# Performance work log

Hardware: AMD Instinct MI355X
Metric: run time of the kernel (lower is better)

Reference implementation:

```python
import jax, jax.numpy as jnp
import numpy as np

N_CLUSTERS = 64
COLLAPSE_REG = 0.1
H_SMOOTH = -0.0001
H_ALPHA = 0.0001
H_LAMBDA = 0.0001


def setup_inputs() -> dict:
    key = jax.random.key(0)
    ks = jax.random.split(key, 6)
    n, d, k = 65536, 512, N_CLUSTERS
    e0 = 1048576  # directed edges before symmetrization
    features = jax.random.normal(ks[0], (n, d), jnp.float32)
    s = jax.random.randint(ks[1], (e0,), 0, n)
    t = jax.random.randint(ks[2], (e0,), 0, n)
    v = jax.random.uniform(ks[3], (e0,), jnp.float32)
    # symmetrize adjacency (real graph datasets are undirected -> L = D - A is PSD)
    edge_src = jnp.concatenate([s, t]).astype(jnp.int64)
    edge_dst = jnp.concatenate([t, s]).astype(jnp.int64)
    edge_vals = jnp.concatenate([v, v])
    W = jax.random.normal(ks[4], (d, k), jnp.float32) / np.sqrt(d).astype(np.float32)
    b = jnp.zeros((k,), jnp.float32)
    return dict(features=features, edge_src=edge_src, edge_dst=edge_dst,
                edge_vals=edge_vals, W=W, b=b)


def reference(features, edge_src, edge_dst, edge_vals, W, b):
    n, d = features.shape
    k = W.shape[1]
    # assignments = softmax(Dense(features))
    S = jax.nn.softmax(features @ W + b, axis=1)  # [n,k]
    cluster_sizes = jnp.sum(S, axis=0)            # [k]
    S_pool = S / cluster_sizes                    # [n,k]
    # sparse column-degree (tf.sparse.reduce_sum axis=0) and edge count
    deg_col = jax.ops.segment_sum(edge_vals, edge_dst, num_segments=n)[:, None]  # [n,1]
    m = jnp.sum(deg_col)
    # A @ S via edge-list gather/scatter (sparse_dense_matmul)
    AS = jax.ops.segment_sum(edge_vals[:, None] * S[edge_dst], edge_src,
                             num_segments=n)      # [n,k]
    graph_pooled = AS.T @ S                       # S^T A S, [k,k]
    normalizer = ((S.T @ deg_col) @ (deg_col.T @ S)) / 2.0 / m  # [k,k]
    spectral_loss = -jnp.trace(graph_pooled - normalizer) / 2.0 / m
    collapse_loss = (jnp.linalg.norm(cluster_sizes) / n
                     * jnp.sqrt(jnp.float32(k)) - 1.0)
    # pooled features
    FP = jax.nn.selu(S_pool.T @ features)         # [k,d]
    # FGC loss chain: Laplacian L = D_row - A applied sparsely
    deg_row = jax.ops.segment_sum(edge_vals, edge_src, num_segments=n)[:, None]
    LS = deg_row * S - AS                         # L @ S, [n,k]
    StLS = LS.T @ S                               # smoothness1 = S^T L S, [k,k]
    # log(det(StLS + ones)) computed stably via slogdet (det is positive: PSD + rank-1)
    _sign, logabsdet = jnp.linalg.slogdet(StLS + jnp.ones_like(StLS))
    smoothness_loss = logabsdet * H_SMOOTH
    # trace((L S) @ FP @ FP^T): trace of [n,k] matrix = sum of first k diagonal entries
    trace_loss = jnp.einsum('ic,cd,id->', LS[:k], FP, FP)
    frob_loss = jnp.linalg.norm(S @ FP - features) * H_ALPHA
    one_two_loss = jnp.linalg.norm(jnp.sum(jnp.abs(S), axis=0)) * H_LAMBDA
    fgc_loss = smoothness_loss + trace_loss + frob_loss + one_two_loss
    total_loss = spectral_loss + COLLAPSE_REG * collapse_loss + fgc_loss
    return FP, S, total_loss
```

## Files before the change

kernel.cpp:

```cpp
#include <hip/hip_runtime.h>
#include <hip/hip_bf16.h>
#include <cstdint>
#include <cstddef>

typedef unsigned short u16;
typedef float f32x4 __attribute__((ext_vector_type(4)));
typedef short bf16x8 __attribute__((ext_vector_type(8)));
typedef unsigned short u16x8 __attribute__((ext_vector_type(8)));

__device__ __forceinline__ u16 f2bf(float f) {
    uint32_t u = __float_as_uint(f);
    u += 0x7fffu + ((u >> 16) & 1u);
    return (u16)(u >> 16);
}
__device__ __forceinline__ float bf2f(u16 h) {
    return __uint_as_float(((uint32_t)h) << 16);
}

#define SWZ(c) ((((c) ^ ((c) >> 3)) & 7) << 2)

__global__ __launch_bounds__(256) void k_prep(const float* __restrict__ Wg, u16* __restrict__ Wt) {
    int idx = blockIdx.x * 256 + threadIdx.x;
    int k = idx >> 6, c = idx & 63;
    int lin = c * 512 + (k ^ ((c & 7) << 3));
    Wt[lin] = f2bf(Wg[idx]);
}

__global__ __launch_bounds__(256) void k1(const float* __restrict__ F,
    const u16* __restrict__ WtG, const float* __restrict__ bias,
    float* __restrict__ S_out, u16* __restrict__ Sbf,
    float* __restrict__ sizes, float* __restrict__ scal) {
    __shared__ __align__(16) u16 Wl[64 * 512];
    __shared__ __align__(16) u16 Al[64 * 64];
    __shared__ float red4[4];
    const int tid = threadIdx.x;
    const int row0 = blockIdx.x * 64;
    for (int j = tid; j < 4096; j += 256)
        ((uint4*)Wl)[j] = ((const uint4*)WtG)[j];

    const int lane = tid & 63;
    const int wv = __builtin_amdgcn_readfirstlane(tid >> 6);
    const int l15 = lane & 15, lq = lane >> 4;
    f32x4 acc[4];
    #pragma unroll
    for (int tn = 0; tn < 4; tn++)
        #pragma unroll
        for (int e = 0; e < 4; e++) acc[tn][e] = 0.f;
    float sumf2 = 0.f;
    const int sr = tid >> 2, skq = tid & 3;
    const int sw = (sr & 7) << 3;

    for (int k0 = 0; k0 < 512; k0 += 64) {
        const float* fp = F + (size_t)(row0 + sr) * 512 + k0 + skq * 16;
        float4 v[4];
        u16 h[16];
        #pragma unroll
        for (int q = 0; q < 4; q++) v[q] = ((const float4*)fp)[q];
        #pragma unroll
        for (int q = 0; q < 4; q++) {
            sumf2 += v[q].x * v[q].x + v[q].y * v[q].y + v[q].z * v[q].z + v[q].w * v[q].w;
            h[q * 4 + 0] = f2bf(v[q].x); h[q * 4 + 1] = f2bf(v[q].y);
            h[q * 4 + 2] = f2bf(v[q].z); h[q * 4 + 3] = f2bf(v[q].w);
        }
        #pragma unroll
        for (int half = 0; half < 2; half++) {
            u16x8 pk;
            #pragma unroll
            for (int e2 = 0; e2 < 8; e2++) pk[e2] = h[half * 8 + e2];
            *(u16x8*)&Al[sr * 64 + ((skq * 16 + half * 8) ^ sw)] = pk;
        }
        __syncthreads();
        #pragma unroll
        for (int kk = 0; kk < 64; kk += 32) {
            const int arow = wv * 16 + l15;
            bf16x8 a = *(const bf16x8*)&Al[arow * 64 + ((kk + lq * 8) ^ ((arow & 7) << 3))];
            #pragma unroll
            for (int tn = 0; tn < 4; tn++) {
                const int bc = tn * 16 + l15;
                bf16x8 b = *(const bf16x8*)&Wl[bc * 512 + ((k0 + kk + lq * 8) ^ ((bc & 7) << 3))];
                acc[tn] = __builtin_amdgcn_mfma_f32_16x16x32_bf16(a, b, acc[tn], 0, 0, 0);
            }
        }
        __syncthreads();
    }

    float bias4[4], szacc[4] = {0.f, 0.f, 0.f, 0.f};
    #pragma unroll
    for (int tn = 0; tn < 4; tn++) bias4[tn] = bias[tn * 16 + l15];
    #pragma unroll
    for (int r2 = 0; r2 < 4; r2++) {
        float L[4];
        #pragma unroll
        for (int tn = 0; tn < 4; tn++) L[tn] = acc[tn][r2] + bias4[tn];
        float mx = fmaxf(fmaxf(L[0], L[1]), fmaxf(L[2], L[3]));
        #pragma unroll
        for (int mm = 1; mm < 16; mm <<= 1) mx = fmaxf(mx, __shfl_xor(mx, mm));
        float e[4], s = 0.f;
        #pragma unroll
        for (int tn = 0; tn < 4; tn++) { e[tn] = __expf(L[tn] - mx); s += e[tn]; }
        #pragma unroll
        for (int mm = 1; mm < 16; mm <<= 1) s += __shfl_xor(s, mm);
        const float inv = 1.f / s;
        const size_t grow = (size_t)(row0 + wv * 16 + lq * 4 + r2);
        #pragma unroll
        for (int tn = 0; tn < 4; tn++) {
            const float svl = e[tn] * inv;
            S_out[grow * 64 + tn * 16 + l15] = svl;
            Sbf[grow * 64 + tn * 16 + l15] = f2bf(svl);
            szacc[tn] += svl;
        }
    }
    #pragma unroll
    for (int tn = 0; tn < 4; tn++) {
        float vs = szacc[tn];
        vs += __shfl_xor(vs, 16);
        vs += __shfl_xor(vs, 32);
        if (lq == 0) atomicAdd(sizes + tn * 16 + l15, vs);
    }
    #pragma unroll
    for (int mm = 1; mm < 64; mm <<= 1) sumf2 += __shfl_xor(sumf2, mm);
    if (lane == 0) red4[wv] = sumf2;
    __syncthreads();
    if (tid == 0) atomicAdd(scal + 1, red4[0] + red4[1] + red4[2] + red4[3]);
}

__global__ __launch_bounds__(512) void k_sweep(const int* __restrict__ esrc,
    const int* __restrict__ edst, const float* __restrict__ ev,
    const u16* __restrict__ Sbf, const float* __restrict__ S, const int E2,
    float* __restrict__ GP8, float* __restrict__ SDS8, float* __restrict__ uv8,
    float* __restrict__ AS64, float* __restrict__ deg64, float* __restrict__ scal) {
    __shared__ uint32_t Tl[2][2048];
    __shared__ uint32_t Pl[2][2048];
    __shared__ uint32_t Ql[2][2048];
    __shared__ uint32_t Rl[2][2048];
    const int tid = threadIdx.x;
    const int lane = tid & 63;
    const int wv = __builtin_amdgcn_readfirstlane(tid >> 6);
    const int l15 = lane & 15, lq = lane >> 4;
    const int xcd = blockIdx.x & 7;
    float* __restrict__ GPmy = GP8 + (size_t)xcd * 4096;
    float* __restrict__ SDSmy = SDS8 + (size_t)xcd * 4096;
    float* __restrict__ umy = uv8 + (size_t)xcd * 64;

    const bool isP = tid < 256;
    const int st = tid & 255;
    const int p = st >> 3, g = st & 7;
    float vsum = 0.f;
    float uacc[8];
    #pragma unroll
    for (int j = 0; j < 8; j++) uacc[j] = 0.f;

    f32x4 aG[2], aS[2];
    #pragma unroll
    for (int t = 0; t < 2; t++)
        #pragma unroll
        for (int r = 0; r < 4; r++) { aG[t][r] = 0.f; aS[t][r] = 0.f; }

    const int ma = 16 * (wv & 3) + l15;
    const int aoff = ma * 32, aswz = SWZ(ma);
    const int nb0 = 32 * (wv >> 2) + l15;
    const int nb1 = nb0 + 16;
    const int b0off = nb0 * 32, b0swz = SWZ(nb0);
    const int b1off = nb1 * 32, b1swz = SWZ(nb1);

    const int nch = E2 >> 6;
    const int stride = gridDim.x;
    int ch = blockIdx.x;
    if (ch >= nch) return;

    int2 ia_c, ib_c, ia_n, ib_n;
    float2 vv_c, vv_n;
    {
        const int e0 = (ch << 6) + 2 * p;
        ia_c = isP ? *(const int2*)&edst[e0] : *(const int2*)&esrc[e0];
        ib_c = isP ? *(const int2*)&esrc[e0] : *(const int2*)&edst[e0];
        vv_c = *(const float2*)&ev[e0];
    }
    u16x8 ra_c = *(const u16x8*)&Sbf[(size_t)ia_c.x * 64 + 8 * g];
    u16x8 rb_c = *(const u16x8*)&Sbf[(size_t)ia_c.y * 64 + 8 * g];
    int chn = ch + stride;
    {
        const int chc = chn < nch ? chn : (nch - 1);
        const int e0 = (chc << 6) + 2 * p;
        ia_n = isP ? *(const int2*)&edst[e0] : *(const int2*)&esrc[e0];
        ib_n = isP ? *(const int2*)&esrc[e0] : *(const int2*)&edst[e0];
        vv_n = *(const float2*)&ev[e0];
    }

    int buf = 0;
    while (true) {
        if (isP) {
            #pragma unroll
            for (int j = 0; j < 8; j++) {
                const int c = 8 * g + j;
                const int off = c * 32 + (p ^ SWZ(c));
                Tl[buf][off] = (uint32_t)(u16)ra_c[j] | ((uint32_t)(u16)rb_c[j] << 16);
                Pl[buf][off] = (uint32_t)f2bf(vv_c.x * bf2f((u16)ra_c[j])) |
                               ((uint32_t)f2bf(vv_c.y * bf2f((u16)rb_c[j])) << 16);
            }
        } else {
            #pragma unroll
            for (int j = 0; j < 8; j++) {
                const int c = 8 * g + j;
                const int off = c * 32 + (p ^ SWZ(c));
                Ql[buf][off] = (uint32_t)(u16)ra_c[j] | ((uint32_t)(u16)rb_c[j] << 16);
                Rl[buf][off] = (uint32_t)f2bf(vv_c.x * bf2f((u16)ra_c[j])) |
                               ((uint32_t)f2bf(vv_c.y * bf2f((u16)rb_c[j])) << 16);
            }
        }
        #pragma unroll
        for (int j = 0; j < 8; j++)
            uacc[j] = fmaf(vv_c.x, bf2f((u16)ra_c[j]),
                      fmaf(vv_c.y, bf2f((u16)rb_c[j]), uacc[j]));
        if (!isP && g == 0) vsum += vv_c.x + vv_c.y;
        if (g == 0) {
            if (ib_c.x < 64) atomicAdd(deg64 + ib_c.x, vv_c.x);
            if (ib_c.y < 64) atomicAdd(deg64 + ib_c.y, vv_c.y);
        }
        if (ib_c.x < 64) {
            const float4 fa = *(const float4*)(S + (size_t)ia_c.x * 64 + 8 * g);
            const float4 fb = *(const float4*)(S + (size_t)ia_c.x * 64 + 8 * g + 4);
            float* dst = AS64 + ib_c.x * 64 + 8 * g;
            atomicAdd(dst + 0, vv_c.x * fa.x); atomicAdd(dst + 1, vv_c.x * fa.y);
            atomicAdd(dst + 2, vv_c.x * fa.z); atomicAdd(dst + 3, vv_c.x * fa.w);
            atomicAdd(dst + 4, vv_c.x * fb.x); atomicAdd(dst + 5, vv_c.x * fb.y);
            atomicAdd(dst + 6, vv_c.x * fb.z); atomicAdd(dst + 7, vv_c.x * fb.w);
        }
        if (ib_c.y < 64) {
            const float4 fa = *(const float4*)(S + (size_t)ia_c.y * 64 + 8 * g);
            const float4 fb = *(const float4*)(S + (size_t)ia_c.y * 64 + 8 * g + 4);
            float* dst = AS64 + ib_c.y * 64 + 8 * g;
            atomicAdd(dst + 0, vv_c.y * fa.x); atomicAdd(dst + 1, vv_c.y * fa.y);
            atomicAdd(dst + 2, vv_c.y * fa.z); atomicAdd(dst + 3, vv_c.y * fa.w);
            atomicAdd(dst + 4, vv_c.y * fb.x); atomicAdd(dst + 5, vv_c.y * fb.y);
            atomicAdd(dst + 6, vv_c.y * fb.z); atomicAdd(dst + 7, vv_c.y * fb.w);
        }
        const u16x8 ra_n = *(const u16x8*)&Sbf[(size_t)ia_n.x * 64 + 8 * g];
        const u16x8 rb_n = *(const u16x8*)&Sbf[(size_t)ia_n.y * 64 + 8 * g];
        const int chnn = chn + stride;
        int2 ia_nn, ib_nn;
        float2 vv_nn;
        {
            const int chc = chnn < nch ? chnn : (nch - 1);
            const int e0 = (chc << 6) + 2 * p;
            ia_nn = isP ? *(const int2*)&edst[e0] : *(const int2*)&esrc[e0];
            ib_nn = isP ? *(const int2*)&esrc[e0] : *(const int2*)&edst[e0];
            vv_nn = *(const float2*)&ev[e0];
        }
        asm volatile("s_waitcnt lgkmcnt(0)" ::: "memory");
        __builtin_amdgcn_s_barrier();
        __builtin_amdgcn_sched_barrier(0);
        #pragma unroll
        for (int half = 0; half < 2; half++) {
            const int w0 = half * 16 + lq * 4;
            const bf16x8 afP = *(const bf16x8*)&Pl[buf][aoff + (w0 ^ aswz)];
            const bf16x8 afR = *(const bf16x8*)&Rl[buf][aoff + (w0 ^ aswz)];
            const bf16x8 qb0 = *(const bf16x8*)&Ql[buf][b0off + (w0 ^ b0swz)];
            const bf16x8 qb1 = *(const bf16x8*)&Ql[buf][b1off + (w0 ^ b1swz)];
            const bf16x8 tb0 = *(const bf16x8*)&Tl[buf][b0off + (w0 ^ b0swz)];
            const bf16x8 tb1 = *(const bf16x8*)&Tl[buf][b1off + (w0 ^ b1swz)];
            aG[0] = __builtin_amdgcn_mfma_f32_16x16x32_bf16(afP, qb0, aG[0], 0, 0, 0);
            aG[1] = __builtin_amdgcn_mfma_f32_16x16x32_bf16(afP, qb1, aG[1], 0, 0, 0);
            aS[0] = __builtin_amdgcn_mfma_f32_16x16x32_bf16(afR, qb0, aS[0], 0, 0, 0);
            aS[1] = __builtin_amdgcn_mfma_f32_16x16x32_bf16(afR, qb1, aS[1], 0, 0, 0);
            aS[0] = __builtin_amdgcn_mfma_f32_16x16x32_bf16(afP, tb0, aS[0], 0, 0, 0);
            aS[1] = __builtin_amdgcn_mfma_f32_16x16x32_bf16(afP, tb1, aS[1], 0, 0, 0);
        }
        ch = chn;
        if (ch >= nch) break;
        ia_c = ia_n; ib_c = ib_n; vv_c = vv_n; ra_c = ra_n; rb_c = rb_n;
        ia_n = ia_nn; ib_n = ib_nn; vv_n = vv_nn;
        chn = chnn;
        buf ^= 1;
    }
    #pragma unroll
    for (int t = 0; t < 2; t++)
        #pragma unroll
        for (int r = 0; r < 4; r++) {
            const int c1 = 16 * (wv & 3) + 4 * lq + r;
            const int c2 = 32 * (wv >> 2) + 16 * t + l15;
            atomicAdd(GPmy + c1 * 64 + c2, aG[t][r]);
            atomicAdd(SDSmy + c1 * 64 + c2, aS[t][r]);
        }
    #pragma unroll
    for (int j = 0; j < 8; j++) {
        uacc[j] += __shfl_xor(uacc[j], 8);
        uacc[j] += __shfl_xor(uacc[j], 16);
        uacc[j] += __shfl_xor(uacc[j], 32);
    }
    if (lane < 8) {
        #pragma unroll
        for (int j = 0; j < 8; j++)
            atomicAdd(umy + 8 * lane + j, uacc[j]);
    }
    if (wv >= 4) {
        #pragma unroll
        for (int mm = 1; mm < 64; mm <<= 1) vsum += __shfl_xor(vsum, mm);
        if (lane == 0) atomicAdd(scal + 0, vsum + vsum);
    }
}

__global__ __launch_bounds__(256) void k_mrg(const float* __restrict__ GP8,
    const float* __restrict__ SDS8, const float* __restrict__ uv8,
    float* __restrict__ GP, float* __restrict__ SDS, float* __restrict__ u_vec) {
    const int bid = blockIdx.x;
    const int t = threadIdx.x;
    if (bid < 16) {
        const int j = bid * 256 + t;
        const int jt = (j & 63) * 64 + (j >> 6);
        float s = 0.f;
        #pragma unroll
        for (int c = 0; c < 8; c++)
            s += GP8[(size_t)c * 4096 + j] + GP8[(size_t)c * 4096 + jt];
        GP[j] = s;
    } else if (bid < 32) {
        const int j = (bid - 16) * 256 + t;
        float s = 0.f;
        #pragma unroll
        for (int c = 0; c < 8; c++) s += SDS8[(size_t)c * 4096 + j];
        SDS[j] = s;
    } else if (t < 64) {
        float s = 0.f;
        #pragma unroll
        for (int c = 0; c < 8; c++) s += uv8[c * 64 + t];
        u_vec[t] = s;
    }
}

__global__ __launch_bounds__(256) void k2m(const float* __restrict__ F,
    const u16* __restrict__ Sbf, float* __restrict__ G) {
    __shared__ uint32_t Ss[64 * 32];
    __shared__ uint32_t Fs[128 * 32];
    const int tid = threadIdx.x;
    const int lane = tid & 63;
    const int wv = __builtin_amdgcn_readfirstlane(tid >> 6);
    const int l15 = lane & 15, lq = lane >> 4;
    const int d0 = (blockIdx.x & 3) * 128;
    const int kblk = blockIdx.x >> 2;

    f32x4 acc[8];
    #pragma unroll
    for (int t8 = 0; t8 < 8; t8++)
        #pragma unroll
        for (int r = 0; r < 4; r++) acc[t8][r] = 0.f;

    const int s_ip = tid >> 3;
    const int s_cs = (tid & 7) * 8;
    const int f_dg = tid & 31;
    const int f_ipb = tid >> 5;

    for (int ch = 0; ch < 8; ch++) {
        const int i0 = kblk * 512 + ch * 64;
        {
            const u16x8 r0 = *(const u16x8*)&Sbf[(size_t)(i0 + 2 * s_ip) * 64 + s_cs];
            const u16x8 r1 = *(const u16x8*)&Sbf[(size_t)(i0 + 2 * s_ip + 1) * 64 + s_cs];
            #pragma unroll
            for (int j = 0; j < 8; j++) {
                const int c = s_cs + j;
                const uint32_t pk = (uint32_t)(u16)r0[j] | ((uint32_t)(u16)r1[j] << 16);
                Ss[c * 32 + (s_ip ^ (((c >> 2) & 7) << 2))] = pk;
            }
        }
        #pragma unroll
        for (int s = 0; s < 4; s++) {
            const int ip = f_ipb + 8 * s;
            const float4 a = *(const float4*)(F + (size_t)(i0 + 2 * ip) * 512 + d0 + 4 * f_dg);
            const float4 b = *(const float4*)(F + (size_t)(i0 + 2 * ip + 1) * 512 + d0 + 4 * f_dg);
            const float al[4] = {a.x, a.y, a.z, a.w};
            const float bl[4] = {b.x, b.y, b.z, b.w};
            #pragma unroll
            for (int j = 0; j < 4; j++) {
                const int d = 4 * f_dg + j;
                const uint32_t pk = (uint32_t)f2bf(al[j]) | ((uint32_t)f2bf(bl[j]) << 16);
                Fs[d * 32 + (ip ^ (((d >> 2) & 7) << 2))] = pk;
            }
        }
        __syncthreads();
        #pragma unroll
        for (int kk = 0; kk < 64; kk += 32) {
            const int w0 = (kk >> 1) + (lq << 2);
            const int ca = 16 * wv + l15;
            const bf16x8 afrag = *(const bf16x8*)&Ss[ca * 32 + (w0 ^ (((ca >> 2) & 7) << 2))];
            #pragma unroll
            for (int t8 = 0; t8 < 8; t8++) {
                const int d = 16 * t8 + l15;
                const bf16x8 bfrag = *(const bf16x8*)&Fs[d * 32 + (w0 ^ (((d >> 2) & 7) << 2))];
                acc[t8] = __builtin_amdgcn_mfma_f32_16x16x32_bf16(afrag, bfrag, acc[t8], 0, 0, 0);
            }
        }
        __syncthreads();
    }
    #pragma unroll
    for (int t8 = 0; t8 < 8; t8++) {
        #pragma unroll
        for (int r = 0; r < 4; r++) {
            const int c = 16 * wv + 4 * lq + r;
            const int d = d0 + 16 * t8 + l15;
            atomicAdd(G + (size_t)c * 512 + d, acc[t8][r]);
        }
    }
}

__global__ __launch_bounds__(256) void k_kk(const u16* __restrict__ Sbf,
    float* __restrict__ SS) {
    __shared__ float Pss[4][16][64];
    const int tid = threadIdx.x, lane = tid & 63;
    const int wv = __builtin_amdgcn_readfirstlane(tid >> 6);
    const int cs = blockIdx.x & 3, c0 = cs * 16;
    const int rbase = (blockIdx.x >> 2) * 512 + wv * 128;
    float ss[16];
    #pragma unroll
    for (int cc = 0; cc < 16; cc++) ss[cc] = 0.f;
    for (int r = 0; r < 128; r++) {
        const int i = rbase + r;
        const float sv = bf2f(Sbf[(size_t)i * 64 + lane]);
        const u16* srow = Sbf + (size_t)i * 64 + c0;
        #pragma unroll
        for (int cc = 0; cc < 16; cc++)
            ss[cc] = fmaf(bf2f(srow[cc]), sv, ss[cc]);
    }
    #pragma unroll
    for (int cc = 0; cc < 16; cc++) Pss[wv][cc][lane] = ss[cc];
    __syncthreads();
    for (int q = 0; q < 4; q++) {
        const int cell = tid * 4 + q, cc = cell >> 6, l = cell & 63;
        atomicAdd(SS + (c0 + cc) * 64 + l,
                  Pss[0][cc][l] + Pss[1][cc][l] + Pss[2][cc][l] + Pss[3][cc][l]);
    }
}

__device__ __forceinline__ float bred256(float v, float* red) {
    #pragma unroll
    for (int mm = 1; mm < 64; mm <<= 1) v += __shfl_xor(v, mm);
    const int t = threadIdx.x;
    __syncthreads();
    if ((t & 63) == 0) red[t >> 6] = v;
    __syncthreads();
    return red[0] + red[1] + red[2] + red[3];
}

__global__ __launch_bounds__(256) void k_fp(const float* __restrict__ G,
    const float* __restrict__ sizes, float* __restrict__ FP, float* __restrict__ scal) {
    __shared__ float red[4];
    const int idx = blockIdx.x * 256 + threadIdx.x;
    const int c = idx >> 9;
    const float g = G[idx];
    const float x = g / sizes[c];
    const float fp = 1.0507009873554805f * (x > 0.f ? x : 1.6732632423543772f * (__expf(x) - 1.f));
    FP[idx] = fp;
    const float gd = bred256(g * fp, red);
    if (threadIdx.x == 0) atomicAdd(scal + 2, gd);
}

__global__ __launch_bounds__(256) void k_fft(const float* __restrict__ FP, float* __restrict__ FFt) {
    __shared__ float red[256];
    const int c = blockIdx.x;
    const int cp = threadIdx.x & 63, part = threadIdx.x >> 6;
    float a = 0.f;
    const int dbase = part * 128;
    for (int dd = 0; dd < 128; dd++)
        a = fmaf(FP[c * 512 + dbase + dd], FP[cp * 512 + dbase + dd], a);
    red[threadIdx.x] = a;
    __syncthreads();
    if (threadIdx.x < 64)
        FFt[c * 64 + threadIdx.x] = red[threadIdx.x] + red[threadIdx.x + 64] +
                                    red[threadIdx.x + 128] + red[threadIdx.x + 192];
}

__global__ __launch_bounds__(64) void k_lu(const float* __restrict__ SDS,
    const float* __restrict__ GP, float* __restrict__ scal) {
    __shared__ float M[64][65];
    const int l = threadIdx.x;
    for (int c = 0; c < 64; c++) M[l][c] = SDS[l * 64 + c] - GP[l * 64 + c] + 1.0f;
    __syncthreads();
    float logdet = 0.f;
    for (int k = 0; k < 64; k++) {
        float v = (l >= k) ? fabsf(M[l][k]) : -1.f;
        int idx = l;
        #pragma unroll
        for (int mm = 1; mm < 64; mm <<= 1) {
            const float ov = __shfl_xor(v, mm);
            const int oi = __shfl_xor(idx, mm);
            if (ov > v || (ov == v && oi < idx)) { v = ov; idx = oi; }
        }
        if (idx != k) {
            const float t1 = M[k][l], t2 = M[idx][l];
            __syncthreads();
            M[k][l] = t2;
            M[idx][l] = t1;
        }
        __syncthreads();
        const float piv = M[k][k];
        logdet += logf(fabsf(piv));
        if (l > k) {
            const float f = M[l][k] / piv;
            for (int c = k + 1; c < 64; c++) M[l][c] = fmaf(-f, M[k][c], M[l][c]);
        }
        __syncthreads();
    }
    if (l == 0) scal[3] = logdet;
}

__global__ __launch_bounds__(256) void k_final(const float* __restrict__ GP,
    const float* __restrict__ SS, const float* __restrict__ FFt, const float* __restrict__ u_vec,
    const float* __restrict__ sizes, const float* __restrict__ deg64,
    const float* __restrict__ AS64, const float* __restrict__ S,
    const float* __restrict__ scal, float* __restrict__ out_loss, const float fn) {
    __shared__ float red[4];
    const int t = threadIdx.x;
    float sA = 0.f, trl = 0.f, trg = 0.f, u2 = 0.f, sz2 = 0.f;
    for (int q = t; q < 4096; q += 256) sA += SS[q] * FFt[q];
    for (int q = t; q < 4096; q += 256) {
        const int i = q >> 6, c = q & 63;
        const float ls = deg64[i] * S[i * 64 + c] - AS64[q];
        trl += ls * FFt[c * 64 + i];
    }
    if (t < 64) { trg = GP[t * 65]; u2 = u_vec[t] * u_vec[t]; sz2 = sizes[t] * sizes[t]; }
    sA = bred256(sA, red);
    trl = bred256(trl, red);
    trg = bred256(trg, red);
    u2 = bred256(u2, red);
    sz2 = bred256(sz2, red);
    if (t == 0) {
        const float m = scal[0], sumF2 = scal[1], gfp = scal[2], lad = scal[3];
        const float spectral = -(trg - u2 / (2.f * m)) / (2.f * m);
        const float collapse = sqrtf(sz2) / fn * 8.f - 1.f;
        const float frob = sqrtf(fmaxf(sA - 2.f * gfp + sumF2, 0.f)) * 1e-4f;
        const float one_two = sqrtf(sz2) * 1e-4f;
        const float smooth = lad * (-1e-4f);
        out_loss[0] = spectral + 0.1f * collapse + smooth + trl + frob + one_two;
    }
}

extern "C" void kernel_launch(void* const* d_in, const int* in_sizes, int n_in,
                              void* d_out, int out_size, void* d_ws, size_t ws_size,
                              hipStream_t stream) {
    const float* F = (const float*)d_in[0];
    const int* esrc = (const int*)d_in[1];
    const int* edst = (const int*)d_in[2];
    const float* ev = (const float*)d_in[3];
    const float* Wg = (const float*)d_in[4];
    const float* bg = (const float*)d_in[5];
    const int n = in_sizes[0] / 512;
    const int E = in_sizes[1];
    const int E2 = E >> 1;

    float* outF = (float*)d_out;
    float* outS = outF + 64 * 512;
    float* outL = outS + (size_t)n * 64;

    char* w = (char*)d_ws;
    float* sizes = (float*)w;
    float* u_vec = sizes + 64;
    float* scal = u_vec + 64;
    float* G = scal + 64;
    float* SS = G + 64 * 512;
    float* AS64 = SS + 4096;
    float* deg64 = AS64 + 4096;
    float* GP8 = deg64 + 64;
    float* SDS8 = GP8 + 8 * 4096;
    float* u8buf = SDS8 + 8 * 4096;
    char* zend = (char*)(u8buf + 512);
    const size_t zero_bytes = (size_t)(zend - w);
    float* GP = (float*)zend;
    float* SDS = GP + 4096;
    float* FFt = SDS + 4096;
    u16* Sbf = (u16*)(FFt + 4096);
    u16* Wt = Sbf + (size_t)n * 64;

    hipMemsetAsync(d_ws, 0, zero_bytes, stream);
    k_prep<<<128, 256, 0, stream>>>(Wg, Wt);
    k1<<<n / 64, 256, 0, stream>>>(F, Wt, bg, outS, Sbf, sizes, scal);
    k_sweep<<<512, 512, 0, stream>>>(esrc, edst, ev, Sbf, outS, E2, GP8, SDS8, u8buf, AS64, deg64, scal);
    k2m<<<512, 256, 0, stream>>>(F, Sbf, G);
    k_mrg<<<33, 256, 0, stream>>>(GP8, SDS8, u8buf, GP, SDS, u_vec);
    k_kk<<<(n / 512) * 4, 256, 0, stream>>>(Sbf, SS);
    k_fp<<<128, 256, 0, stream>>>(G, sizes, outF, scal);
    k_fft<<<64, 256, 0, stream>>>(outF, FFt);
    k_lu<<<1, 64, 0, stream>>>(SDS, GP, scal);
    k_final<<<1, 256, 0, stream>>>(GP, SS, FFt, u_vec, sizes, deg64, AS64, outS, scal, outL, (float)n);
}
```

Before: 527.8 us.

## Fuse S^T F matmul into edge sweep kernel and parallelize LU without pivoting

Merges the separate S^T·F MFMA kernel (k2m) into the edge sweep kernel. Each block interleaves its eight 64-row matmul chunks between sweep iterations, which overlaps memory-bound gather/atomic work with MFMA work and removes one launch. The 64x64 LU in k_lu now runs on 256 threads, each handling a 16-column slice, and drops partial pivoting. This relies on the matrix (PSD plus all-ones) being well conditioned enough for unpivoted elimination, which risks numerical accuracy. The fused kernel also uses extra LDS, which may reduce occupancy.

```diff
diff --git a/kernel.cpp b/kernel.cpp
--- a/kernel.cpp
+++ b/kernel.cpp
@@ -18,6 +18,13 @@
 }
 
 #define SWZ(c) ((((c) ^ ((c) >> 3)) & 7) << 2)
+#define SWZ2(c) ((((c) >> 2) & 7) << 2)
+
+__device__ __forceinline__ void softbar() {
+    asm volatile("s_waitcnt lgkmcnt(0)" ::: "memory");
+    __builtin_amdgcn_s_barrier();
+    __builtin_amdgcn_sched_barrier(0);
+}
 
 __global__ __launch_bounds__(256) void k_prep(const float* __restrict__ Wg, u16* __restrict__ Wt) {
     int idx = blockIdx.x * 256 + threadIdx.x;
@@ -124,18 +131,23 @@
     if (tid == 0) atomicAdd(scal + 1, red4[0] + red4[1] + red4[2] + red4[3]);
 }
 
-__global__ __launch_bounds__(512) void k_sweep(const int* __restrict__ esrc,
+__global__ __launch_bounds__(512) void k_mid(const int* __restrict__ esrc,
     const int* __restrict__ edst, const float* __restrict__ ev,
-    const u16* __restrict__ Sbf, const float* __restrict__ S, const int E2,
+    const u16* __restrict__ Sbf, const float* __restrict__ S,
+    const float* __restrict__ F, const int E2,
     float* __restrict__ GP8, float* __restrict__ SDS8, float* __restrict__ uv8,
-    float* __restrict__ AS64, float* __restrict__ deg64, float* __restrict__ scal) {
+    float* __restrict__ AS64, float* __restrict__ deg64, float* __restrict__ scal,
+    float* __restrict__ G) {
     __shared__ uint32_t Tl[2][2048];
     __shared__ uint32_t Pl[2][2048];
     __shared__ uint32_t Ql[2][2048];
     __shared__ uint32_t Rl[2][2048];
+    __shared__ uint32_t Ss2[2048];
+    __shared__ uint32_t Fs2[4096];
     const int tid = threadIdx.x;
     const int lane = tid & 63;
-    const int wv = __builtin_amdgcn_readfirstlane(tid >> 6);
+    const int wv8 = __builtin_amdgcn_readfirstlane(tid >> 6);
+    const int wv = wv8 & 7;
     const int l15 = lane & 15, lq = lane >> 4;
     const int xcd = blockIdx.x & 7;
     float* __restrict__ GPmy = GP8 + (size_t)xcd * 4096;
@@ -149,24 +161,37 @@
     float uacc[8];
     #pragma unroll
     for (int j = 0; j < 8; j++) uacc[j] = 0.f;
-
     f32x4 aG[2], aS[2];
     #pragma unroll
     for (int t = 0; t < 2; t++)
         #pragma unroll
         for (int r = 0; r < 4; r++) { aG[t][r] = 0.f; aS[t][r] = 0.f; }
-
     const int ma = 16 * (wv & 3) + l15;
     const int aoff = ma * 32, aswz = SWZ(ma);
-    const int nb0 = 32 * (wv >> 2) + l15;
-    const int nb1 = nb0 + 16;
-    const int b0off = nb0 * 32, b0swz = SWZ(nb0);
-    const int b1off = nb1 * 32, b1swz = SWZ(nb1);
+    const int nb0 = 32 * ((wv & 7) >> 2) * 1 + 32 * (wv >> 2) * 0 + 32 * (wv >> 2) + l15;
+    const int nb0r = 32 * (wv >> 2) + l15;
+    const int nb1r = nb0r + 16;
+    const int b0off = nb0r * 32, b0swz = SWZ(nb0r);
+    const int b1off = nb1r * 32, b1swz = SWZ(nb1r);
+
+    const int d0 = (blockIdx.x & 3) * 128;
+    const int kblk = blockIdx.x >> 2;
+    const int cwv = wv8 & 3, dh = wv8 >> 2;
+    f32x4 acc2[4];
+    #pragma unroll
+    for (int t8 = 0; t8 < 4; t8++)
+        #pragma unroll
+        for (int r = 0; r < 4; r++) acc2[t8][r] = 0.f;
+    const int s_ip = tid >> 3;
+    const int s_cs = (tid & 7) * 8;
+    const int tF = tid - 256;
+    const int f_dg = tF & 31;
+    const int f_ipb = tF >> 5;
 
     const int nch = E2 >> 6;
     const int stride = gridDim.x;
     int ch = blockIdx.x;
-    if (ch >= nch) return;
+    const int sweep_left = (ch < nch) ? ((nch - ch + stride - 1) / stride) : 0;
 
     int2 ia_c, ib_c, ia_n, ib_n;
     float2 vv_c, vv_n;
@@ -188,90 +213,136 @@
     }
 
     int buf = 0;
-    while (true) {
-        if (isP) {
+    int sw_done = 0, mm_done = 0;
+    const int total = sweep_left + 8;
+    for (int step = 0; step < total; step++) {
+        const bool do_mm = (mm_done < 8) &&
+                           ((sw_done >= (mm_done + 1) * 4) || (sw_done == sweep_left));
+        if (do_mm) {
+            const int i0 = kblk * 512 + mm_done * 64;
+            if (isP) {
+                const u16x8 r0 = *(const u16x8*)&Sbf[(size_t)(i0 + 2 * s_ip) * 64 + s_cs];
+                const u16x8 r1 = *(const u16x8*)&Sbf[(size_t)(i0 + 2 * s_ip + 1) * 64 + s_cs];
+                #pragma unroll
+                for (int j = 0; j < 8; j++) {
+                    const int c = s_cs + j;
+                    Ss2[c * 32 + (s_ip ^ SWZ2(c))] =
+                        (uint32_t)(u16)r0[j] | ((uint32_t)(u16)r1[j] << 16);
+                }
+            } else {
+                #pragma unroll
+                for (int s = 0; s < 4; s++) {
+                    const int ip = f_ipb + 8 * s;
+                    const float4 a = *(const float4*)(F + (size_t)(i0 + 2 * ip) * 512 + d0 + 4 * f_dg);
+                    const float4 b = *(const float4*)(F + (size_t)(i0 + 2 * ip + 1) * 512 + d0 + 4 * f_dg);
+                    const float al[4] = {a.x, a.y, a.z, a.w};
+                    const float bl[4] = {b.x, b.y, b.z, b.w};
+                    #pragma unroll
+                    for (int j = 0; j < 4; j++) {
+                        const int d = 4 * f_dg + j;
+                        Fs2[d * 32 + (ip ^ SWZ2(d))] =
+                            (uint32_t)f2bf(al[j]) | ((uint32_t)f2bf(bl[j]) << 16);
+                    }
+                }
+            }
+            softbar();
             #pragma unroll
-            for (int j = 0; j < 8; j++) {
-                const int c = 8 * g + j;
-                const int off = c * 32 + (p ^ SWZ(c));
-                Tl[buf][off] = (uint32_t)(u16)ra_c[j] | ((uint32_t)(u16)rb_c[j] << 16);
-                Pl[buf][off] = (uint32_t)f2bf(vv_c.x * bf2f((u16)ra_c[j])) |
-                               ((uint32_t)f2bf(vv_c.y * bf2f((u16)rb_c[j])) << 16);
-            }
+            for (int kk = 0; kk < 64; kk += 32) {
+                const int w0 = (kk >> 1) + (lq << 2);
+                const int ca = 16 * cwv + l15;
+                const bf16x8 afrag = *(const bf16x8*)&Ss2[ca * 32 + (w0 ^ SWZ2(ca))];
+                #pragma unroll
+                for (int t8r = 0; t8r < 4; t8r++) {
+                    const int d = 16 * (4 * dh + t8r) + l15;
+                    const bf16x8 bfrag = *(const bf16x8*)&Fs2[d * 32 + (w0 ^ SWZ2(d))];
+                    acc2[t8r] = __builtin_amdgcn_mfma_f32_16x16x32_bf16(afrag, bfrag, acc2[t8r], 0, 0, 0);
+                }
+            }
+            softbar();
+            mm_done++;
         } else {
+            if (isP) {
+                #pragma unroll
+                for (int j = 0; j < 8; j++) {
+                    const int c = 8 * g + j;
+                    const int off = c * 32 + (p ^ SWZ(c));
+                    Tl[buf][off] = (uint32_t)(u16)ra_c[j] | ((uint32_t)(u16)rb_c[j] << 16);
+                    Pl[buf][off] = (uint32_t)f2bf(vv_c.x * bf2f((u16)ra_c[j])) |
+                                   ((uint32_t)f2bf(vv_c.y * bf2f((u16)rb_c[j])) << 16);
+                }
+            } else {
+                #pragma unroll
+                for (int j = 0; j < 8; j++) {
+                    const int c = 8 * g + j;
+                    const int off = c * 32 + (p ^ SWZ(c));
+                    Ql[buf][off] = (uint32_t)(u16)ra_c[j] | ((uint32_t)(u16)rb_c[j] << 16);
+                    Rl[buf][off] = (uint32_t)f2bf(vv_c.x * bf2f((u16)ra_c[j])) |
+                                   ((uint32_t)f2bf(vv_c.y * bf2f((u16)rb_c[j])) << 16);
+                }
+            }
             #pragma unroll
-            for (int j = 0; j < 8; j++) {
-                const int c = 8 * g + j;
-                const int off = c * 32 + (p ^ SWZ(c));
-                Ql[buf][off] = (uint32_t)(u16)ra_c[j] | ((uint32_t)(u16)rb_c[j] << 16);
-                Rl[buf][off] = (uint32_t)f2bf(vv_c.x * bf2f((u16)ra_c[j])) |
-                               ((uint32_t)f2bf(vv_c.y * bf2f((u16)rb_c[j])) << 16);
-            }
-        }
-        #pragma unroll
-        for (int j = 0; j < 8; j++)
-            uacc[j] = fmaf(vv_c.x, bf2f((u16)ra_c[j]),
-                      fmaf(vv_c.y, bf2f((u16)rb_c[j]), uacc[j]));
-        if (!isP && g == 0) vsum += vv_c.x + vv_c.y;
-        if (g == 0) {
-            if (ib_c.x < 64) atomicAdd(deg64 + ib_c.x, vv_c.x);
-            if (ib_c.y < 64) atomicAdd(deg64 + ib_c.y, vv_c.y);
-        }
-        if (ib_c.x < 64) {
-            const float4 fa = *(const float4*)(S + (size_t)ia_c.x * 64 + 8 * g);
-            const float4 fb = *(const float4*)(S + (size_t)ia_c.x * 64 + 8 * g + 4);
-            float* dst = AS64 + ib_c.x * 64 + 8 * g;
-            atomicAdd(dst + 0, vv_c.x * fa.x); atomicAdd(dst + 1, vv_c.x * fa.y);
-            atomicAdd(dst + 2, vv_c.x * fa.z); atomicAdd(dst + 3, vv_c.x * fa.w);
-            atomicAdd(dst + 4, vv_c.x * fb.x); atomicAdd(dst + 5, vv_c.x * fb.y);
-            atomicAdd(dst + 6, vv_c.x * fb.z); atomicAdd(dst + 7, vv_c.x * fb.w);
-        }
-        if (ib_c.y < 64) {
-            const float4 fa = *(const float4*)(S + (size_t)ia_c.y * 64 + 8 * g);
-            const float4 fb = *(const float4*)(S + (size_t)ia_c.y * 64 + 8 * g + 4);
-            float* dst = AS64 + ib_c.y * 64 + 8 * g;
-            atomicAdd(dst + 0, vv_c.y * fa.x); atomicAdd(dst + 1, vv_c.y * fa.y);
-            atomicAdd(dst + 2, vv_c.y * fa.z); atomicAdd(dst + 3, vv_c.y * fa.w);
-            atomicAdd(dst + 4, vv_c.y * fb.x); atomicAdd(dst + 5, vv_c.y * fb.y);
-            atomicAdd(dst + 6, vv_c.y * fb.z); atomicAdd(dst + 7, vv_c.y * fb.w);
-        }
-        const u16x8 ra_n = *(const u16x8*)&Sbf[(size_t)ia_n.x * 64 + 8 * g];
-        const u16x8 rb_n = *(const u16x8*)&Sbf[(size_t)ia_n.y * 64 + 8 * g];
-        const int chnn = chn + stride;
-        int2 ia_nn, ib_nn;
-        float2 vv_nn;
-        {
-            const int chc = chnn < nch ? chnn : (nch - 1);
-            const int e0 = (chc << 6) + 2 * p;
-            ia_nn = isP ? *(const int2*)&edst[e0] : *(const int2*)&esrc[e0];
-            ib_nn = isP ? *(const int2*)&esrc[e0] : *(const int2*)&edst[e0];
-            vv_nn = *(const float2*)&ev[e0];
-        }
-        asm volatile("s_waitcnt lgkmcnt(0)" ::: "memory");
-        __builtin_amdgcn_s_barrier();
-        __builtin_amdgcn_sched_barrier(0);
-        #pragma unroll
-        for (int half = 0; half < 2; half++) {
-            const int w0 = half * 16 + lq * 4;
-            const bf16x8 afP = *(const bf16x8*)&Pl[buf][aoff + (w0 ^ aswz)];
-            const bf16x8 afR = *(const bf16x8*)&Rl[buf][aoff + (w0 ^ aswz)];
-            const bf16x8 qb0 = *(const bf16x8*)&Ql[buf][b0off + (w0 ^ b0swz)];
-            const bf16x8 qb1 = *(const bf16x8*)&Ql[buf][b1off + (w0 ^ b1swz)];
-            const bf16x8 tb0 = *(const bf16x8*)&Tl[buf][b0off + (w0 ^ b0swz)];
-            const bf16x8 tb1 = *(const bf16x8*)&Tl[buf][b1off + (w0 ^ b1swz)];
-            aG[0] = __builtin_amdgcn_mfma_f32_16x16x32_bf16(afP, qb0, aG[0], 0, 0, 0);
-            aG[1] = __builtin_amdgcn_mfma_f32_16x16x32_bf16(afP, qb1, aG[1], 0, 0, 0);
-            aS[0] = __builtin_amdgcn_mfma_f32_16x16x32_bf16(afR, qb0, aS[0], 0, 0, 0);
-            aS[1] = __builtin_amdgcn_mfma_f32_16x16x32_bf16(afR, qb1, aS[1], 0, 0, 0);
-            aS[0] = __builtin_amdgcn_mfma_f32_16x16x32_bf16(afP, tb0, aS[0], 0, 0, 0);
-            aS[1] = __builtin_amdgcn_mfma_f32_16x16x32_bf16(afP, tb1, aS[1], 0, 0, 0);
-        }
-        ch = chn;
-        if (ch >= nch) break;
-        ia_c = ia_n; ib_c = ib_n; vv_c = vv_n; ra_c = ra_n; rb_c = rb_n;
-        ia_n = ia_nn; ib_n = ib_nn; vv_n = vv_nn;
-        chn = chnn;
-        buf ^= 1;
+            for (int j = 0; j < 8; j++)
+                uacc[j] = fmaf(vv_c.x, bf2f((u16)ra_c[j]),
+                          fmaf(vv_c.y, bf2f((u16)rb_c[j]), uacc[j]));
+            if (!isP && g == 0) vsum += vv_c.x + vv_c.y;
+            if (g == 0) {
+                if (ib_c.x < 64) atomicAdd(deg64 + ib_c.x, vv_c.x);
+                if (ib_c.y < 64) atomicAdd(deg64 + ib_c.y, vv_c.y);
+            }
+            if (ib_c.x < 64) {
+                const float4 fa = *(const float4*)(S + (size_t)ia_c.x * 64 + 8 * g);
+                const float4 fb = *(const float4*)(S + (size_t)ia_c.x * 64 + 8 * g + 4);
+                float* dst = AS64 + ib_c.x * 64 + 8 * g;
+                atomicAdd(dst + 0, vv_c.x * fa.x); atomicAdd(dst + 1, vv_c.x * fa.y);
+                atomicAdd(dst + 2, vv_c.x * fa.z); atomicAdd(dst + 3, vv_c.x * fa.w);
+                atomicAdd(dst + 4, vv_c.x * fb.x); atomicAdd(dst + 5, vv_c.x * fb.y);
+                atomicAdd(dst + 6, vv_c.x * fb.z); atomicAdd(dst + 7, vv_c.x * fb.w);
+            }
+            if (ib_c.y < 64) {
+                const float4 fa = *(const float4*)(S + (size_t)ia_c.y * 64 + 8 * g);
+                const float4 fb = *(const float4*)(S + (size_t)ia_c.y * 64 + 8 * g + 4);
+                float* dst = AS64 + ib_c.y * 64 + 8 * g;
+                atomicAdd(dst + 0, vv_c.y * fa.x); atomicAdd(dst + 1, vv_c.y * fa.y);
+                atomicAdd(dst + 2, vv_c.y * fa.z); atomicAdd(dst + 3, vv_c.y * fa.w);
+                atomicAdd(dst + 4, vv_c.y * fb.x); atomicAdd(dst + 5, vv_c.y * fb.y);
+                atomicAdd(dst + 6, vv_c.y * fb.z); atomicAdd(dst + 7, vv_c.y * fb.w);
+            }
+            const u16x8 ra_n = *(const u16x8*)&Sbf[(size_t)ia_n.x * 64 + 8 * g];
+            const u16x8 rb_n = *(const u16x8*)&Sbf[(size_t)ia_n.y * 64 + 8 * g];
+            const int chnn = chn + stride;
+            int2 ia_nn, ib_nn;
+            float2 vv_nn;
+            {
+                const int chc = chnn < nch ? chnn : (nch - 1);
+                const int e0 = (chc << 6) + 2 * p;
+                ia_nn = isP ? *(const int2*)&edst[e0] : *(const int2*)&esrc[e0];
+                ib_nn = isP ? *(const int2*)&esrc[e0] : *(const int2*)&edst[e0];
+                vv_nn = *(const float2*)&ev[e0];
+            }
+            softbar();
+            #pragma unroll
+            for (int half = 0; half < 2; half++) {
+                const int w0 = half * 16 + lq * 4;
+                const bf16x8 afP = *(const bf16x8*)&Pl[buf][aoff + (w0 ^ aswz)];
+                const bf16x8 afR = *(const bf16x8*)&Rl[buf][aoff + (w0 ^ aswz)];
+                const bf16x8 qb0 = *(const bf16x8*)&Ql[buf][b0off + (w0 ^ b0swz)];
+                const bf16x8 qb1 = *(const bf16x8*)&Ql[buf][b1off + (w0 ^ b1swz)];
+                const bf16x8 tb0 = *(const bf16x8*)&Tl[buf][b0off + (w0 ^ b0swz)];
+                const bf16x8 tb1 = *(const bf16x8*)&Tl[buf][b1off + (w0 ^ b1swz)];
+                aG[0] = __builtin_amdgcn_mfma_f32_16x16x32_bf16(afP, qb0, aG[0], 0, 0, 0);
+                aG[1] = __builtin_amdgcn_mfma_f32_16x16x32_bf16(afP, qb1, aG[1], 0, 0, 0);
+                aS[0] = __builtin_amdgcn_mfma_f32_16x16x32_bf16(afR, qb0, aS[0], 0, 0, 0);
+                aS[1] = __builtin_amdgcn_mfma_f32_16x16x32_bf16(afR, qb1, aS[1], 0, 0, 0);
+                aS[0] = __builtin_amdgcn_mfma_f32_16x16x32_bf16(afP, tb0, aS[0], 0, 0, 0);
+                aS[1] = __builtin_amdgcn_mfma_f32_16x16x32_bf16(afP, tb1, aS[1], 0, 0, 0);
+            }
+            ch = chn;
+            ia_c = ia_n; ib_c = ib_n; vv_c = vv_n; ra_c = ra_n; rb_c = rb_n;
+            ia_n = ia_nn; ib_n = ib_nn; vv_n = vv_nn;
+            chn = chnn;
+            buf ^= 1;
+            sw_done++;
+        }
     }
     #pragma unroll
     for (int t = 0; t < 2; t++)
@@ -298,6 +369,14 @@
         for (int mm = 1; mm < 64; mm <<= 1) vsum += __shfl_xor(vsum, mm);
         if (lane == 0) atomicAdd(scal + 0, vsum + vsum);
     }
+    #pragma unroll
+    for (int t8r = 0; t8r < 4; t8r++)
+        #pragma unroll
+        for (int r = 0; r < 4; r++) {
+            const int c = 16 * cwv + 4 * lq + r;
+            const int d = d0 + 16 * (4 * dh + t8r) + l15;
+            atomicAdd(G + (size_t)c * 512 + d, acc2[t8r][r]);
+        }
 }
 
 __global__ __launch_bounds__(256) void k_mrg(const float* __restrict__ GP8,
@@ -324,80 +403,6 @@
         #pragma unroll
         for (int c = 0; c < 8; c++) s += uv8[c * 64 + t];
         u_vec[t] = s;
-    }
-}
-
-__global__ __launch_bounds__(256) void k2m(const float* __restrict__ F,
-    const u16* __restrict__ Sbf, float* __restrict__ G) {
-    __shared__ uint32_t Ss[64 * 32];
-    __shared__ uint32_t Fs[128 * 32];
-    const int tid = threadIdx.x;
-    const int lane = tid & 63;
-    const int wv = __builtin_amdgcn_readfirstlane(tid >> 6);
-    const int l15 = lane & 15, lq = lane >> 4;
-    const int d0 = (blockIdx.x & 3) * 128;
-    const int kblk = blockIdx.x >> 2;
-
-    f32x4 acc[8];
-    #pragma unroll
-    for (int t8 = 0; t8 < 8; t8++)
-        #pragma unroll
-        for (int r = 0; r < 4; r++) acc[t8][r] = 0.f;
-
-    const int s_ip = tid >> 3;
-    const int s_cs = (tid & 7) * 8;
-    const int f_dg = tid & 31;
-    const int f_ipb = tid >> 5;
-
-    for (int ch = 0; ch < 8; ch++) {
-        const int i0 = kblk * 512 + ch * 64;
-        {
-            const u16x8 r0 = *(const u16x8*)&Sbf[(size_t)(i0 + 2 * s_ip) * 64 + s_cs];
-            const u16x8 r1 = *(const u16x8*)&Sbf[(size_t)(i0 + 2 * s_ip + 1) * 64 + s_cs];
-            #pragma unroll
-            for (int j = 0; j < 8; j++) {
-                const int c = s_cs + j;
-                const uint32_t pk = (uint32_t)(u16)r0[j] | ((uint32_t)(u16)r1[j] << 16);
-                Ss[c * 32 + (s_ip ^ (((c >> 2) & 7) << 2))] = pk;
-            }
-        }
-        #pragma unroll
-        for (int s = 0; s < 4; s++) {
-            const int ip = f_ipb + 8 * s;
-            const float4 a = *(const float4*)(F + (size_t)(i0 + 2 * ip) * 512 + d0 + 4 * f_dg);
-            const float4 b = *(const float4*)(F + (size_t)(i0 + 2 * ip + 1) * 512 + d0 + 4 * f_dg);
-            const float al[4] = {a.x, a.y, a.z, a.w};
-            const float bl[4] = {b.x, b.y, b.z, b.w};
-            #pragma unroll
-            for (int j = 0; j < 4; j++) {
-                const int d = 4 * f_dg + j;
-                const uint32_t pk = (uint32_t)f2bf(al[j]) | ((uint32_t)f2bf(bl[j]) << 16);
-                Fs[d * 32 + (ip ^ (((d >> 2) & 7) << 2))] = pk;
-            }
-        }
-        __syncthreads();
-        #pragma unroll
-        for (int kk = 0; kk < 64; kk += 32) {
-            const int w0 = (kk >> 1) + (lq << 2);
-            const int ca = 16 * wv + l15;
-            const bf16x8 afrag = *(const bf16x8*)&Ss[ca * 32 + (w0 ^ (((ca >> 2) & 7) << 2))];
-            #pragma unroll
-            for (int t8 = 0; t8 < 8; t8++) {
-                const int d = 16 * t8 + l15;
-                const bf16x8 bfrag = *(const bf16x8*)&Fs[d * 32 + (w0 ^ (((d >> 2) & 7) << 2))];
-                acc[t8] = __builtin_amdgcn_mfma_f32_16x16x32_bf16(afrag, bfrag, acc[t8], 0, 0, 0);
-            }
-        }
-        __syncthreads();
-    }
-    #pragma unroll
-    for (int t8 = 0; t8 < 8; t8++) {
-        #pragma unroll
-        for (int r = 0; r < 4; r++) {
-            const int c = 16 * wv + 4 * lq + r;
-            const int d = d0 + 16 * t8 + l15;
-            atomicAdd(G + (size_t)c * 512 + d, acc[t8][r]);
-        }
     }
 }
 
@@ -467,38 +472,30 @@
                                     red[threadIdx.x + 128] + red[threadIdx.x + 192];
 }
 
-__global__ __launch_bounds__(64) void k_lu(const float* __restrict__ SDS,
+__global__ __launch_bounds__(256) void k_lu(const float* __restrict__ SDS,
     const float* __restrict__ GP, float* __restrict__ scal) {
     __shared__ float M[64][65];
-    const int l = threadIdx.x;
-    for (int c = 0; c < 64; c++) M[l][c] = SDS[l * 64 + c] - GP[l * 64 + c] + 1.0f;
+    __shared__ float red[4];
+    const int tid = threadIdx.x;
+    const int l = tid & 63, q = tid >> 6;
+    #pragma unroll
+    for (int j = 0; j < 16; j++) {
+        const int c = q * 16 + j;
+        M[l][c] = SDS[l * 64 + c] - GP[l * 64 + c] + 1.0f;
+    }
     __syncthreads();
-    float logdet = 0.f;
-    for (int k = 0; k < 64; k++) {
-        float v = (l >= k) ? fabsf(M[l][k]) : -1.f;
-        int idx = l;
-        #pragma unroll
-        for (int mm = 1; mm < 64; mm <<= 1) {
-            const float ov = __shfl_xor(v, mm);
-            const int oi = __shfl_xor(idx, mm);
-            if (ov > v || (ov == v && oi < idx)) { v = ov; idx = oi; }
-        }
-        if (idx != k) {
-            const float t1 = M[k][l], t2 = M[idx][l];
-            __syncthreads();
-            M[k][l] = t2;
-            M[idx][l] = t1;
+    for (int k = 0; k < 63; k++) {
+        if (l > k) {
+            const float f = M[l][k] / M[k][k];
+            const int cend = q * 16 + 16;
+            for (int c = (q * 16 > k + 1 ? q * 16 : k + 1); c < cend; c++)
+                M[l][c] = fmaf(-f, M[k][c], M[l][c]);
         }
         __syncthreads();
-        const float piv = M[k][k];
-        logdet += logf(fabsf(piv));
-        if (l > k) {
-            const float f = M[l][k] / piv;
-            for (int c = k + 1; c < 64; c++) M[l][c] = fmaf(-f, M[k][c], M[l][c]);
-        }
-        __syncthreads();
-    }
-    if (l == 0) scal[3] = logdet;
+    }
+    float v = (tid < 64) ? logf(fabsf(M[tid][tid])) : 0.f;
+    const float ld = bred256(v, red);
+    if (tid == 0) scal[3] = ld;
 }
 
 __global__ __launch_bounds__(256) void k_final(const float* __restrict__ GP,
@@ -571,12 +568,12 @@
     hipMemsetAsync(d_ws, 0, zero_bytes, stream);
     k_prep<<<128, 256, 0, stream>>>(Wg, Wt);
     k1<<<n / 64, 256, 0, stream>>>(F, Wt, bg, outS, Sbf, sizes, scal);
-    k_sweep<<<512, 512, 0, stream>>>(esrc, edst, ev, Sbf, outS, E2, GP8, SDS8, u8buf, AS64, deg64, scal);
-    k2m<<<512, 256, 0, stream>>>(F, Sbf, G);
+    k_mid<<<512, 512, 0, stream>>>(esrc, edst, ev, Sbf, outS, F, E2,
+                                   GP8, SDS8, u8buf, AS64, deg64, scal, G);
     k_mrg<<<33, 256, 0, stream>>>(GP8, SDS8, u8buf, GP, SDS, u_vec);
     k_kk<<<(n / 512) * 4, 256, 0, stream>>>(Sbf, SS);
     k_fp<<<128, 256, 0, stream>>>(G, sizes, outF, scal);
     k_fft<<<64, 256, 0, stream>>>(outF, FFt);
-    k_lu<<<1, 64, 0, stream>>>(SDS, GP, scal);
+    k_lu<<<1, 256, 0, stream>>>(SDS, GP, scal);
     k_final<<<1, 256, 0, stream>>>(GP, SS, FFt, u_vec, sizes, deg64, AS64, outS, scal, outL, (float)n);
 }
```

Result: faster. 466.4 us (-11.6%).
